# Optimization experiments

Measured on AMD Instinct MI355X. Metric: run time of the kernel, lower is better.

## Reference

```python
import jax, jax.numpy as jnp
import numpy as np

D_MODEL = 256
D_STATE = 2
BATCH = 8
SEQ = 8192


def setup_inputs() -> dict:
    key = jax.random.key(0)
    ks = jax.random.split(key, 8)
    s = 1.0 / np.sqrt(D_STATE)
    x = jax.random.normal(ks[0], (BATCH, SEQ, D_MODEL), dtype=jnp.float32)
    # stable range so exp(cumsum) stays finite at T=8192 (see notes)
    log_a_mag = -jax.random.uniform(ks[1], (D_MODEL, D_STATE), jnp.float32, 1e-5, 1e-3)
    a_phase = jax.random.uniform(ks[2], (D_MODEL, D_STATE), jnp.float32, 0.0, 2.0 * np.pi)
    B_re = jax.random.normal(ks[3], (D_MODEL, D_STATE), jnp.float32) * s
    B_im = jax.random.normal(ks[4], (D_MODEL, D_STATE), jnp.float32) * s
    C_re = jax.random.normal(ks[5], (D_MODEL, D_STATE), jnp.float32) * s
    C_im = jax.random.normal(ks[6], (D_MODEL, D_STATE), jnp.float32) * s
    D_diag = jnp.ones((D_MODEL,), jnp.float32)
    return dict(x=x, log_a_mag=log_a_mag, a_phase=a_phase, B_re=B_re, B_im=B_im,
                C_re=C_re, C_im=C_im, D_diag=D_diag)


def reference(x, log_a_mag, a_phase, B_re, B_im, C_re, C_im, D_diag):
    # x: (B, T, D); params: (D, S)
    Bsz, T, D = x.shape
    S = log_a_mag.shape[1]
    # cumulative complex log-decay along time, shape (D, S, T)
    cum_r = jnp.cumsum(jnp.broadcast_to(log_a_mag[:, :, None], (D, S, T)), axis=-1)
    cum_i = jnp.cumsum(jnp.broadcast_to(a_phase[:, :, None], (D, S, T)), axis=-1)
    x_t = jnp.swapaxes(x, 1, 2)                      # (B, D, T)
    Bu_r = B_re[None, :, :, None] * x_t[:, :, None, :]   # (B, D, S, T)
    Bu_i = B_im[None, :, :, None] * x_t[:, :, None, :]
    # exp(-cum_log_a): descale inputs
    en = jnp.exp(-cum_r)
    enr = en * jnp.cos(-cum_i)
    eni = en * jnp.sin(-cum_i)
    sr = enr * Bu_r - eni * Bu_i
    si = enr * Bu_i + eni * Bu_r
    csr = jnp.cumsum(sr, axis=-1)
    csi = jnp.cumsum(si, axis=-1)
    # exp(+cum_log_a): rescale prefix sums -> hidden states h (B, D, S, T)
    ec = jnp.exp(cum_r)
    ecr = ec * jnp.cos(cum_i)
    eci = ec * jnp.sin(cum_i)
    h_r = ecr * csr - eci * csi
    h_i = ecr * csi + eci * csr
    # output: Re(C . h) summed over state + skip D*x
    y = jnp.einsum('bdst,ds->bdt', h_r, C_re) - jnp.einsum('bdst,ds->bdt', h_i, C_im)
    y = jnp.swapaxes(y, 1, 2) + D_diag * x           # (B, T, D)
    return y
```

## Files before the change

### kernel.cpp

```cpp
#include <hip/hip_runtime.h>
#include <math.h>

#define BATCH  8
#define SEQ    8192
#define DMODEL 256
#define DSTATE 2


__global__ void ssm_chunk_state(const float* __restrict__ x,
                                const float* __restrict__ lam,
                                const float* __restrict__ aph,
                                const float* __restrict__ Bre,
                                const float* __restrict__ Bim,
                                float* __restrict__ E,
                                int C, int L) {
    const int lane = threadIdx.x;
    const int bid  = blockIdx.x;
    const int b = bid / C;
    const int c = bid % C;
    const int d0 = lane * 4;

    float ar[4][2], ai[4][2], br[4][2], bi[4][2];
#pragma unroll
    for (int j = 0; j < 4; ++j) {
        const int d = d0 + j;
#pragma unroll
        for (int s = 0; s < 2; ++s) {
            const float lm = lam[d * 2 + s];
            const float ph = aph[d * 2 + s];
            const float m  = expf(lm);
            ar[j][s] = m * cosf(ph);
            ai[j][s] = m * sinf(ph);
            br[j][s] = Bre[d * 2 + s];
            bi[j][s] = Bim[d * 2 + s];
        }
    }

    float hr[4][2] = {}, hi[4][2] = {};

    const float* xp = x + ((size_t)b * SEQ + (size_t)c * L) * DMODEL + d0;
#pragma unroll 4
    for (int t = 0; t < L; ++t) {
        const float4 xv = *reinterpret_cast<const float4*>(xp + (size_t)t * DMODEL);
        const float xj[4] = {xv.x, xv.y, xv.z, xv.w};
#pragma unroll
        for (int j = 0; j < 4; ++j) {
#pragma unroll
            for (int s = 0; s < 2; ++s) {
                const float nr = fmaf(ar[j][s], hr[j][s],
                                 fmaf(-ai[j][s], hi[j][s], br[j][s] * xj[j]));
                const float ni = fmaf(ar[j][s], hi[j][s],
                                 fmaf( ai[j][s], hr[j][s], bi[j][s] * xj[j]));
                hr[j][s] = nr;
                hi[j][s] = ni;
            }
        }
    }

    float* ep = E + ((size_t)(b * C + c) * 64 + lane) * 16;
#pragma unroll
    for (int j = 0; j < 4; ++j) {
        float4 v;
        v.x = hr[j][0]; v.y = hi[j][0];
        v.z = hr[j][1]; v.w = hi[j][1];
        reinterpret_cast<float4*>(ep)[j] = v;
    }
}

__global__ void ssm_chunk_scan(const float* __restrict__ E,
                               float* __restrict__ Hin,
                               const float* __restrict__ lam,
                               const float* __restrict__ aph,
                               int C, int L) {
    const int g = blockIdx.x * blockDim.x + threadIdx.x;
    const int b = g >> 9;
    const int r = g & 511;
    const int d4 = r >> 3;
    const int j  = (r >> 1) & 3;
    const int s  = r & 1;
    const int d  = d4 * 4 + j;

    const double l = (double)lam[d * 2 + s] * (double)L;
    const double p = (double)aph[d * 2 + s] * (double)L;
    const double m = exp(l);
    const float aLr = (float)(m * cos(p));
    const float aLi = (float)(m * sin(p));

    const size_t base = (size_t)b * C * 1024 + (size_t)r * 2;

    float hr = 0.f, hi = 0.f;
#pragma unroll 4
    for (int c = 0; c < C; ++c) {
        const size_t off = base + (size_t)c * 1024;
        const float2 e = *reinterpret_cast<const float2*>(E + off);
        *reinterpret_cast<float2*>(Hin + off) = make_float2(hr, hi);
        const float nr = fmaf(aLr, hr, fmaf(-aLi, hi, e.x));
        const float ni = fmaf(aLr, hi, fmaf( aLi, hr, e.y));
        hr = nr;
        hi = ni;
    }
}

__global__ void ssm_output(const float* __restrict__ x,
                           const float* __restrict__ lam,
                           const float* __restrict__ aph,
                           const float* __restrict__ Bre,
                           const float* __restrict__ Bim,
                           const float* __restrict__ Cre,
                           const float* __restrict__ Cim,
                           const float* __restrict__ Dd,
                           const float* __restrict__ Hin,
                           float* __restrict__ y,
                           int C, int L) {
    const int lane = threadIdx.x;
    const int bid  = blockIdx.x;
    const int b = bid / C;
    const int c = bid % C;
    const int d0 = lane * 4;

    float ar[4][2], ai[4][2], br[4][2], bi[4][2], cr[4][2], ci[4][2], dd[4];
#pragma unroll
    for (int j = 0; j < 4; ++j) {
        const int d = d0 + j;
        dd[j] = Dd[d];
#pragma unroll
        for (int s = 0; s < 2; ++s) {
            const float lm = lam[d * 2 + s];
            const float ph = aph[d * 2 + s];
            const float m  = expf(lm);
            ar[j][s] = m * cosf(ph);
            ai[j][s] = m * sinf(ph);
            br[j][s] = Bre[d * 2 + s];
            bi[j][s] = Bim[d * 2 + s];
            cr[j][s] = Cre[d * 2 + s];
            ci[j][s] = Cim[d * 2 + s];
        }
    }

    float hr[4][2], hi[4][2];
    const float* hp = Hin + ((size_t)(b * C + c) * 64 + lane) * 16;
#pragma unroll
    for (int j = 0; j < 4; ++j) {
        const float4 v = reinterpret_cast<const float4*>(hp)[j];
        hr[j][0] = v.x; hi[j][0] = v.y;
        hr[j][1] = v.z; hi[j][1] = v.w;
    }

    const size_t tbase = ((size_t)b * SEQ + (size_t)c * L) * DMODEL + d0;
    const float* xp = x + tbase;
    float* yp = y + tbase;
#pragma unroll 4
    for (int t = 0; t < L; ++t) {
        const float4 xv = *reinterpret_cast<const float4*>(xp + (size_t)t * DMODEL);
        const float xj[4] = {xv.x, xv.y, xv.z, xv.w};
        float yj[4];
#pragma unroll
        for (int j = 0; j < 4; ++j) {
            float acc = dd[j] * xj[j];
#pragma unroll
            for (int s = 0; s < 2; ++s) {
                const float nr = fmaf(ar[j][s], hr[j][s],
                                 fmaf(-ai[j][s], hi[j][s], br[j][s] * xj[j]));
                const float ni = fmaf(ar[j][s], hi[j][s],
                                 fmaf( ai[j][s], hr[j][s], bi[j][s] * xj[j]));
                hr[j][s] = nr;
                hi[j][s] = ni;
                acc = fmaf(cr[j][s], nr, acc);
                acc = fmaf(-ci[j][s], ni, acc);
            }
            yj[j] = acc;
        }
        float4 yv;
        yv.x = yj[0]; yv.y = yj[1]; yv.z = yj[2]; yv.w = yj[3];
        *reinterpret_cast<float4*>(yp + (size_t)t * DMODEL) = yv;
    }
}

extern "C" void kernel_launch(void* const* d_in, const int* in_sizes, int n_in,
                              void* d_out, int out_size, void* d_ws, size_t ws_size,
                              hipStream_t stream) {
    const float* x   = (const float*)d_in[0];
    const float* lam = (const float*)d_in[1];
    const float* aph = (const float*)d_in[2];
    const float* Bre = (const float*)d_in[3];
    const float* Bim = (const float*)d_in[4];
    const float* Cre = (const float*)d_in[5];
    const float* Cim = (const float*)d_in[6];
    const float* Dd  = (const float*)d_in[7];
    float* y = (float*)d_out;

    int C = 256;
    while (C > 8 && ws_size < (size_t)2 * BATCH * C * 1024 * sizeof(float)) C >>= 1;
    const int L = SEQ / C;

    float* E   = (float*)d_ws;
    float* Hin = E + (size_t)BATCH * C * 1024;

    ssm_chunk_state<<<BATCH * C, 64, 0, stream>>>(x, lam, aph, Bre, Bim, E, C, L);
    ssm_chunk_scan<<<(BATCH * DMODEL * DSTATE) / 256, 256, 0, stream>>>(E, Hin, lam, aph, C, L);
    ssm_output<<<BATCH * C, 64, 0, stream>>>(x, lam, aph, Bre, Bim, Cre, Cim, Dd, Hin, y, C, L);
}
```

Measured before the change: 179.2 us.

## Parallelize cross-chunk scan with wavefront shuffle prefix scan over chunks

Replaces the serial per-(batch,state) loop over 256 chunks in the middle kernel with a wavefront-wide parallel scan. Each of 64 lanes handles 4 chunks and combines them with shuffle-up steps using precomputed decay powers, which shortens the sequential dependency chain from 256 to about 10 steps. Chunk count and length become compile-time constants, dropping the workspace-size fallback. This assumes the workspace always holds 256 chunks and adds double-precision exp/sincos per scan step.

```diff
diff --git a/kernel.cpp b/kernel.cpp
--- a/kernel.cpp
+++ b/kernel.cpp
@@ -5,6 +5,8 @@
 #define SEQ    8192
 #define DMODEL 256
 #define DSTATE 2
+#define CHUNKS 256
+#define CLEN   32
 
 
 __global__ void ssm_chunk_state(const float* __restrict__ x,
@@ -12,12 +14,11 @@
                                 const float* __restrict__ aph,
                                 const float* __restrict__ Bre,
                                 const float* __restrict__ Bim,
-                                float* __restrict__ E,
-                                int C, int L) {
+                                float* __restrict__ E) {
     const int lane = threadIdx.x;
     const int bid  = blockIdx.x;
-    const int b = bid / C;
-    const int c = bid % C;
+    const int b = bid / CHUNKS;
+    const int c = bid % CHUNKS;
     const int d0 = lane * 4;
 
     float ar[4][2], ai[4][2], br[4][2], bi[4][2];
@@ -38,9 +39,9 @@
 
     float hr[4][2] = {}, hi[4][2] = {};
 
-    const float* xp = x + ((size_t)b * SEQ + (size_t)c * L) * DMODEL + d0;
+    const float* xp = x + ((size_t)b * SEQ + (size_t)c * CLEN) * DMODEL + d0;
 #pragma unroll 4
-    for (int t = 0; t < L; ++t) {
+    for (int t = 0; t < CLEN; ++t) {
         const float4 xv = *reinterpret_cast<const float4*>(xp + (size_t)t * DMODEL);
         const float xj[4] = {xv.x, xv.y, xv.z, xv.w};
 #pragma unroll
@@ -57,7 +58,7 @@
         }
     }
 
-    float* ep = E + ((size_t)(b * C + c) * 64 + lane) * 16;
+    float* ep = E + ((size_t)(b * CHUNKS + c) * 64 + lane) * 16;
 #pragma unroll
     for (int j = 0; j < 4; ++j) {
         float4 v;
@@ -70,34 +71,67 @@
 __global__ void ssm_chunk_scan(const float* __restrict__ E,
                                float* __restrict__ Hin,
                                const float* __restrict__ lam,
-                               const float* __restrict__ aph,
-                               int C, int L) {
-    const int g = blockIdx.x * blockDim.x + threadIdx.x;
+                               const float* __restrict__ aph) {
+    const int lane = threadIdx.x & 63;
+    const int g = blockIdx.x * 4 + (threadIdx.x >> 6);
     const int b = g >> 9;
     const int r = g & 511;
-    const int d4 = r >> 3;
-    const int j  = (r >> 1) & 3;
-    const int s  = r & 1;
-    const int d  = d4 * 4 + j;
-
-    const double l = (double)lam[d * 2 + s] * (double)L;
-    const double p = (double)aph[d * 2 + s] * (double)L;
-    const double m = exp(l);
-    const float aLr = (float)(m * cos(p));
-    const float aLi = (float)(m * sin(p));
-
-    const size_t base = (size_t)b * C * 1024 + (size_t)r * 2;
-
-    float hr = 0.f, hi = 0.f;
-#pragma unroll 4
-    for (int c = 0; c < C; ++c) {
-        const size_t off = base + (size_t)c * 1024;
-        const float2 e = *reinterpret_cast<const float2*>(E + off);
-        *reinterpret_cast<float2*>(Hin + off) = make_float2(hr, hi);
-        const float nr = fmaf(aLr, hr, fmaf(-aLi, hi, e.x));
-        const float ni = fmaf(aLr, hi, fmaf( aLi, hr, e.y));
-        hr = nr;
-        hi = ni;
+    const int d = (r >> 3) * 4 + ((r >> 1) & 3);
+    const int s = r & 1;
+
+    const double lm = (double)lam[d * 2 + s];
+    const double ph = (double)aph[d * 2 + s];
+    {
+    }
+    const double mL = exp(lm * (double)CLEN);
+    const double pL = ph * (double)CLEN;
+    const float Ar = (float)(mL * cos(pL));
+    const float Ai = (float)(mL * sin(pL));
+
+    const size_t base = (size_t)b * CHUNKS * 1024 + (size_t)r * 2;
+
+    float2 e[4];
+#pragma unroll
+    for (int i = 0; i < 4; ++i) {
+        const int c = lane * 4 + i;
+        e[i] = *reinterpret_cast<const float2*>(E + base + (size_t)c * 1024);
+    }
+
+    float vr = e[0].x, vi = e[0].y;
+#pragma unroll
+    for (int i = 1; i < 4; ++i) {
+        const float nr = fmaf(Ar, vr, fmaf(-Ai, vi, e[i].x));
+        const float ni = fmaf(Ar, vi, fmaf( Ai, vr, e[i].y));
+        vr = nr; vi = ni;
+    }
+
+#pragma unroll
+    for (int st = 0; st < 6; ++st) {
+        const int k = 1 << st;
+        const double n = (double)CLEN * 4.0 * (double)k;
+        const double mm = exp(lm * n);
+        const double pp = ph * n;
+        const float Wr = (float)(mm * cos(pp));
+        const float Wi = (float)(mm * sin(pp));
+        const float ur = __shfl_up(vr, (unsigned)k);
+        const float ui = __shfl_up(vi, (unsigned)k);
+        if (lane >= k) {
+            vr = fmaf(Wr, ur, fmaf(-Wi, ui, vr));
+            vi = fmaf(Wr, ui, fmaf( Wi, ur, vi));
+        }
+    }
+
+    float pr = __shfl_up(vr, 1);
+    float pi = __shfl_up(vi, 1);
+    if (lane == 0) { pr = 0.f; pi = 0.f; }
+
+#pragma unroll
+    for (int i = 0; i < 4; ++i) {
+        const int c = lane * 4 + i;
+        *reinterpret_cast<float2*>(Hin + base + (size_t)c * 1024) = make_float2(pr, pi);
+        const float nr = fmaf(Ar, pr, fmaf(-Ai, pi, e[i].x));
+        const float ni = fmaf(Ar, pi, fmaf( Ai, pr, e[i].y));
+        pr = nr; pi = ni;
     }
 }
 
@@ -110,12 +144,11 @@
                            const float* __restrict__ Cim,
                            const float* __restrict__ Dd,
                            const float* __restrict__ Hin,
-                           float* __restrict__ y,
-                           int C, int L) {
+                           float* __restrict__ y) {
     const int lane = threadIdx.x;
     const int bid  = blockIdx.x;
-    const int b = bid / C;
-    const int c = bid % C;
+    const int b = bid / CHUNKS;
+    const int c = bid % CHUNKS;
     const int d0 = lane * 4;
 
     float ar[4][2], ai[4][2], br[4][2], bi[4][2], cr[4][2], ci[4][2], dd[4];
@@ -138,7 +171,7 @@
     }
 
     float hr[4][2], hi[4][2];
-    const float* hp = Hin + ((size_t)(b * C + c) * 64 + lane) * 16;
+    const float* hp = Hin + ((size_t)(b * CHUNKS + c) * 64 + lane) * 16;
 #pragma unroll
     for (int j = 0; j < 4; ++j) {
         const float4 v = reinterpret_cast<const float4*>(hp)[j];
@@ -146,11 +179,11 @@
         hr[j][1] = v.z; hi[j][1] = v.w;
     }
 
-    const size_t tbase = ((size_t)b * SEQ + (size_t)c * L) * DMODEL + d0;
+    const size_t tbase = ((size_t)b * SEQ + (size_t)c * CLEN) * DMODEL + d0;
     const float* xp = x + tbase;
     float* yp = y + tbase;
 #pragma unroll 4
-    for (int t = 0; t < L; ++t) {
+    for (int t = 0; t < CLEN; ++t) {
         const float4 xv = *reinterpret_cast<const float4*>(xp + (size_t)t * DMODEL);
         const float xj[4] = {xv.x, xv.y, xv.z, xv.w};
         float yj[4];
@@ -189,14 +222,10 @@
     const float* Dd  = (const float*)d_in[7];
     float* y = (float*)d_out;
 
-    int C = 256;
-    while (C > 8 && ws_size < (size_t)2 * BATCH * C * 1024 * sizeof(float)) C >>= 1;
-    const int L = SEQ / C;
-
     float* E   = (float*)d_ws;
-    float* Hin = E + (size_t)BATCH * C * 1024;
-
-    ssm_chunk_state<<<BATCH * C, 64, 0, stream>>>(x, lam, aph, Bre, Bim, E, C, L);
-    ssm_chunk_scan<<<(BATCH * DMODEL * DSTATE) / 256, 256, 0, stream>>>(E, Hin, lam, aph, C, L);
-    ssm_output<<<BATCH * C, 64, 0, stream>>>(x, lam, aph, Bre, Bim, Cre, Cim, Dd, Hin, y, C, L);
-}
+    float* Hin = E + (size_t)BATCH * CHUNKS * 1024;
+
+    ssm_chunk_state<<<BATCH * CHUNKS, 64, 0, stream>>>(x, lam, aph, Bre, Bim, E);
+    ssm_chunk_scan<<<(BATCH * 512) / 4, 256, 0, stream>>>(E, Hin, lam, aph);
+    ssm_output<<<BATCH * CHUNKS, 64, 0, stream>>>(x, lam, aph, Bre, Bim, Cre, Cim, Dd, Hin, y);
+}
```

Measured after the change: 170.3 us. -5.0%, faster.
